# Kernel optimization log

Hardware: AMD Instinct MI355X
Metric: run time of the kernel (lower is better)

Reference implementation:

```python
import jax, jax.numpy as jnp
import numpy as np

N_NODES = 50000
N_EDGES = 600000
D = 128
EPS = 1e-5


def setup_inputs() -> dict:
    key = jax.random.key(0)
    ks = jax.random.split(key, 12)
    s = 1.0 / np.sqrt(D)
    return {
        "h": jax.random.normal(ks[0], (N_NODES, D), dtype=jnp.float32),
        "src": jax.random.randint(ks[1], (N_EDGES,), 0, N_NODES),
        "dst": jax.random.randint(ks[2], (N_EDGES,), 0, N_NODES),
        "W_pre": jax.random.uniform(ks[3], (D, D), jnp.float32, -s, s),
        "b_pre": jax.random.uniform(ks[4], (D,), jnp.float32, -s, s),
        "W1": jax.random.uniform(ks[5], (D, D), jnp.float32, -s, s),
        "b1": jax.random.uniform(ks[6], (D,), jnp.float32, -s, s),
        "W2": jax.random.uniform(ks[7], (D, D), jnp.float32, -s, s),
        "b2": jax.random.uniform(ks[8], (D,), jnp.float32, -s, s),
        "gamma": jnp.ones((D,), jnp.float32),
        "beta": jnp.zeros((D,), jnp.float32),
    }


def layer_norm(x, gamma, beta):
    mu = jnp.mean(x, axis=-1, keepdims=True)
    var = jnp.mean(jnp.square(x - mu), axis=-1, keepdims=True)
    return (x - mu) * jax.lax.rsqrt(var + EPS) * gamma + beta


def reference(h, src, dst, W_pre, b_pre, W1, b1, W2, b2, gamma, beta):
    # pre-projection: [N, D]
    h = h @ W_pre + b_pre
    # message passing: gather from src, segment-sum at dst (copy_u + sum)
    agg = jax.ops.segment_sum(h[src], dst, num_segments=N_NODES)
    # MLP (dropout is identity in eval)
    h_new = jax.nn.relu(jax.nn.relu(agg @ W1 + b1) @ W2 + b2)
    # residual + LayerNorm
    return layer_norm(h + h_new, gamma, beta)
```

## Files before the change

### kernel.cpp

```cpp
#include <hip/hip_runtime.h>

#define D 128
#define EPS 1e-5f
#define SCAN_CHUNK 1024
#define TSTRIDE 136

typedef __attribute__((ext_vector_type(8))) short bf16x8;
typedef __attribute__((ext_vector_type(4))) float floatx4;

__device__ __forceinline__ unsigned short f2bf(float f) {
    union { float f; unsigned u; } v; v.f = f;
    unsigned r = v.u + 0x7fffu + ((v.u >> 16) & 1u);
    return (unsigned short)(r >> 16);
}
__device__ __forceinline__ float bf2f(unsigned short s) {
    union { unsigned u; float f; } v; v.u = ((unsigned)s) << 16; return v.f;
}

__global__ __launch_bounds__(256) void prep(const float* __restrict__ W0,
                                            const float* __restrict__ W1,
                                            const float* __restrict__ W2,
                                            unsigned short* __restrict__ wt,
                                            int* __restrict__ counts, int nN) {
    int idx = blockIdx.x * 256 + threadIdx.x;
    if (idx < 3 * D * D) {
        int w = idx >> 14;
        int r = idx & (D * D - 1);
        int f = r >> 7, k = r & (D - 1);
        const float* W = (w == 0) ? W0 : (w == 1) ? W1 : W2;
        wt[(size_t)w * D * D + (size_t)f * D + k] = f2bf(W[(size_t)k * D + f]);
    }
    if (idx < nN) counts[idx] = 0;
}

__global__ __launch_bounds__(256) void hist_dst(const int* __restrict__ dst,
                                                int* __restrict__ counts, int nE) {
    int e = blockIdx.x * 256 + threadIdx.x;
    if (e < nE) atomicAdd(&counts[dst[e]], 1);
}

__global__ __launch_bounds__(256) void scan_chunk_sums(const int* __restrict__ counts,
                                                       int* __restrict__ chunkSums, int n) {
    __shared__ int sh[256];
    const int t = threadIdx.x;
    const int base = blockIdx.x * SCAN_CHUNK + t * 4;
    int s = 0;
#pragma unroll
    for (int i = 0; i < 4; ++i) {
        int idx = base + i;
        if (idx < n) s += counts[idx];
    }
    sh[t] = s;
    __syncthreads();
    for (int off = 128; off > 0; off >>= 1) {
        if (t < off) sh[t] += sh[t + off];
        __syncthreads();
    }
    if (t == 0) chunkSums[blockIdx.x] = sh[0];
}

__global__ __launch_bounds__(64) void scan_top(int* __restrict__ chunkSums, int nChunks,
                                               int* __restrict__ offsets, int nN, int nE) {
    const int t = threadIdx.x;
    int orig = (t < nChunks) ? chunkSums[t] : 0;
    int v = orig;
#pragma unroll
    for (int off = 1; off < 64; off <<= 1) {
        int u = __shfl_up(v, off, 64);
        if (t >= off) v += u;
    }
    if (t < nChunks) chunkSums[t] = v - orig;
    if (t == 0) offsets[nN] = nE;
}

__global__ __launch_bounds__(256) void scan_final(const int* __restrict__ counts,
                                                  const int* __restrict__ chunkSums,
                                                  int* __restrict__ offsets,
                                                  int* __restrict__ cursor, int n) {
    __shared__ int sh[256];
    const int t = threadIdx.x;
    const int base = blockIdx.x * SCAN_CHUNK + t * 4;
    int c[4];
    int s = 0;
#pragma unroll
    for (int i = 0; i < 4; ++i) {
        int idx = base + i;
        c[i] = (idx < n) ? counts[idx] : 0;
        s += c[i];
    }
    sh[t] = s;
    __syncthreads();
    int val = s;
    for (int off = 1; off < 256; off <<= 1) {
        int u = (t >= off) ? sh[t - off] : 0;
        __syncthreads();
        val += u;
        sh[t] = val;
        __syncthreads();
    }
    int run = val - s + chunkSums[blockIdx.x];
#pragma unroll
    for (int i = 0; i < 4; ++i) {
        int idx = base + i;
        if (idx < n) {
            offsets[idx] = run;
            cursor[idx] = run;
        }
        run += c[i];
    }
}

__global__ __launch_bounds__(256) void fill_edges(const int* __restrict__ src,
                                                  const int* __restrict__ dst,
                                                  int* __restrict__ cursor,
                                                  int* __restrict__ edge_src, int nE) {
    int e = blockIdx.x * 256 + threadIdx.x;
    if (e < nE) {
        int pos = atomicAdd(&cursor[dst[e]], 1);
        edge_src[pos] = src[e];
    }
}

__global__ __launch_bounds__(256) void gemm1(const float* __restrict__ X,
                                             const unsigned short* __restrict__ Wt,
                                             const float* __restrict__ bias,
                                             unsigned short* __restrict__ Y, int nrows) {
    const int t = threadIdx.x;
    const int lane = t & 63, wave = t >> 6;
    const int g = wave >> 1, hf = wave & 1;
    const int ml = lane & 15, q = lane >> 4;
    const int node = blockIdx.x * 32 + g * 16 + ml;
    const int rr = (node < nrows) ? node : (nrows - 1);
    const bool ok = (node < nrows);

    bf16x8 bfrag[4];
    const float* xp = X + (size_t)rr * D + q * 8;
#pragma unroll
    for (int kb = 0; kb < 4; ++kb) {
        float4 f0 = *(const float4*)(xp + kb * 32);
        float4 f1 = *(const float4*)(xp + kb * 32 + 4);
        bf16x8 v;
        v[0] = (short)f2bf(f0.x); v[1] = (short)f2bf(f0.y);
        v[2] = (short)f2bf(f0.z); v[3] = (short)f2bf(f0.w);
        v[4] = (short)f2bf(f1.x); v[5] = (short)f2bf(f1.y);
        v[6] = (short)f2bf(f1.z); v[7] = (short)f2bf(f1.w);
        bfrag[kb] = v;
    }

#pragma unroll
    for (int tl2 = 0; tl2 < 4; ++tl2) {
        const int tl = hf * 4 + tl2;
        floatx4 acc = {0.f, 0.f, 0.f, 0.f};
        const unsigned short* wp = Wt + (size_t)(tl * 16 + ml) * D + q * 8;
#pragma unroll
        for (int kb = 0; kb < 4; ++kb) {
            bf16x8 af = *(const bf16x8*)(wp + kb * 32);
            acc = __builtin_amdgcn_mfma_f32_16x16x32_bf16(af, bfrag[kb], acc, 0, 0, 0);
        }
        const int f0i = tl * 16 + q * 4;
        float4 b4 = *(const float4*)(bias + f0i);
        if (ok) {
            ushort4 o;
            o.x = f2bf(acc[0] + b4.x); o.y = f2bf(acc[1] + b4.y);
            o.z = f2bf(acc[2] + b4.z); o.w = f2bf(acc[3] + b4.w);
            *(ushort4*)(Y + (size_t)node * D + f0i) = o;
        }
    }
}

__global__ __launch_bounds__(256) void gather_sum(const unsigned short* __restrict__ hpre,
                                                  const int* __restrict__ offsets,
                                                  const int* __restrict__ edge_src,
                                                  unsigned short* __restrict__ agg, int nN) {
    const int t = threadIdx.x;
    const int li = t & 15;
    const int n = blockIdx.x * 16 + (t >> 4);
    if (n >= nN) return;
    const int beg = offsets[n], end = offsets[n + 1];

    float a[8] = {0.f, 0.f, 0.f, 0.f, 0.f, 0.f, 0.f, 0.f};
    int j = beg;
    int s0 = 0, s1 = 0;
    if (j < end) s0 = edge_src[j];
    if (j + 1 < end) s1 = edge_src[j + 1];

    while (j + 1 < end) {
        const int c0 = s0, c1 = s1;
        const int jn = j + 2;
        if (jn < end) s0 = edge_src[jn];
        if (jn + 1 < end) s1 = edge_src[jn + 1];
        bf16x8 v0 = *(const bf16x8*)(hpre + (size_t)c0 * D + li * 8);
        bf16x8 v1 = *(const bf16x8*)(hpre + (size_t)c1 * D + li * 8);
#pragma unroll
        for (int i = 0; i < 8; ++i)
            a[i] += bf2f((unsigned short)v0[i]) + bf2f((unsigned short)v1[i]);
        j = jn;
    }
    if (j < end) {
        bf16x8 v0 = *(const bf16x8*)(hpre + (size_t)s0 * D + li * 8);
#pragma unroll
        for (int i = 0; i < 8; ++i) a[i] += bf2f((unsigned short)v0[i]);
    }

    bf16x8 p;
#pragma unroll
    for (int i = 0; i < 8; ++i) p[i] = (short)f2bf(a[i]);
    *(bf16x8*)(agg + (size_t)n * D + li * 8) = p;
}

__global__ __launch_bounds__(256) void fused_mlp(const unsigned short* __restrict__ agg,
                                                 const unsigned short* __restrict__ hpre,
                                                 const unsigned short* __restrict__ Wt1,
                                                 const float* __restrict__ b1,
                                                 const unsigned short* __restrict__ Wt2,
                                                 const float* __restrict__ b2,
                                                 const float* __restrict__ gamma,
                                                 const float* __restrict__ beta,
                                                 float* __restrict__ out, int nN) {
    __shared__ unsigned short tile[32 * TSTRIDE];
    __shared__ float psm[2][32], psq[2][32];
    const int t = threadIdx.x;
    const int lane = t & 63, wave = t >> 6;
    const int g = wave >> 1, hf = wave & 1;
    const int ml = lane & 15, q = lane >> 4;
    const int lr = g * 16 + ml;
    const int node = blockIdx.x * 32 + lr;
    const int rr = (node < nN) ? node : (nN - 1);
    const bool ok = (node < nN);

    {
        bf16x8 bfrag[4];
        const unsigned short* xp = agg + (size_t)rr * D + q * 8;
#pragma unroll
        for (int kb = 0; kb < 4; ++kb) bfrag[kb] = *(const bf16x8*)(xp + kb * 32);

#pragma unroll
        for (int tl2 = 0; tl2 < 4; ++tl2) {
            const int tl = hf * 4 + tl2;
            floatx4 acc = {0.f, 0.f, 0.f, 0.f};
            const unsigned short* wp = Wt1 + (size_t)(tl * 16 + ml) * D + q * 8;
#pragma unroll
            for (int kb = 0; kb < 4; ++kb) {
                bf16x8 af = *(const bf16x8*)(wp + kb * 32);
                acc = __builtin_amdgcn_mfma_f32_16x16x32_bf16(af, bfrag[kb], acc, 0, 0, 0);
            }
            const int f0i = tl * 16 + q * 4;
            float4 b4 = *(const float4*)(b1 + f0i);
            ushort4 o;
            o.x = f2bf(fmaxf(acc[0] + b4.x, 0.f));
            o.y = f2bf(fmaxf(acc[1] + b4.y, 0.f));
            o.z = f2bf(fmaxf(acc[2] + b4.z, 0.f));
            o.w = f2bf(fmaxf(acc[3] + b4.w, 0.f));
            *(ushort4*)(&tile[lr * TSTRIDE + f0i]) = o;
        }
    }
    __syncthreads();

    float vs[4][4];
    float sm = 0.f, sq = 0.f;
    {
        bf16x8 bfrag[4];
#pragma unroll
        for (int kb = 0; kb < 4; ++kb)
            bfrag[kb] = *(const bf16x8*)(&tile[lr * TSTRIDE + kb * 32 + q * 8]);

#pragma unroll
        for (int tl2 = 0; tl2 < 4; ++tl2) {
            const int tl = hf * 4 + tl2;
            floatx4 acc = {0.f, 0.f, 0.f, 0.f};
            const unsigned short* wp = Wt2 + (size_t)(tl * 16 + ml) * D + q * 8;
#pragma unroll
            for (int kb = 0; kb < 4; ++kb) {
                bf16x8 af = *(const bf16x8*)(wp + kb * 32);
                acc = __builtin_amdgcn_mfma_f32_16x16x32_bf16(af, bfrag[kb], acc, 0, 0, 0);
            }
            const int f0i = tl * 16 + q * 4;
            float4 b4 = *(const float4*)(b2 + f0i);
            ushort4 hr = ((const ushort4*)(hpre + (size_t)rr * D + f0i))[0];
            float a0 = fmaxf(acc[0] + b4.x, 0.f) + bf2f(hr.x);
            float a1 = fmaxf(acc[1] + b4.y, 0.f) + bf2f(hr.y);
            float a2 = fmaxf(acc[2] + b4.z, 0.f) + bf2f(hr.z);
            float a3 = fmaxf(acc[3] + b4.w, 0.f) + bf2f(hr.w);
            vs[tl2][0] = a0; vs[tl2][1] = a1; vs[tl2][2] = a2; vs[tl2][3] = a3;
            sm += a0 + a1 + a2 + a3;
            sq += a0 * a0 + a1 * a1 + a2 * a2 + a3 * a3;
        }
        sm += __shfl_xor(sm, 16); sm += __shfl_xor(sm, 32);
        sq += __shfl_xor(sq, 16); sq += __shfl_xor(sq, 32);
        if (lane < 16) { psm[hf][lr] = sm; psq[hf][lr] = sq; }
    }
    __syncthreads();

    {
        const float smT = psm[0][lr] + psm[1][lr];
        const float sqT = psq[0][lr] + psq[1][lr];
        const float mu = smT * (1.f / D);
        const float var = sqT * (1.f / D) - mu * mu;
        const float is = rsqrtf(var + EPS);

        if (ok) {
#pragma unroll
            for (int tl2 = 0; tl2 < 4; ++tl2) {
                const int f0i = (hf * 4 + tl2) * 16 + q * 4;
                float4 g4 = *(const float4*)(gamma + f0i);
                float4 be4 = *(const float4*)(beta + f0i);
                float4 o;
                o.x = (vs[tl2][0] - mu) * is * g4.x + be4.x;
                o.y = (vs[tl2][1] - mu) * is * g4.y + be4.y;
                o.z = (vs[tl2][2] - mu) * is * g4.z + be4.z;
                o.w = (vs[tl2][3] - mu) * is * g4.w + be4.w;
                *(float4*)(out + (size_t)node * D + f0i) = o;
            }
        }
    }
}

extern "C" void kernel_launch(void* const* d_in, const int* in_sizes, int n_in,
                              void* d_out, int out_size, void* d_ws, size_t ws_size,
                              hipStream_t stream) {
    const float* h     = (const float*)d_in[0];
    const int*   src   = (const int*)d_in[1];
    const int*   dst   = (const int*)d_in[2];
    const float* W_pre = (const float*)d_in[3];
    const float* b_pre = (const float*)d_in[4];
    const float* W1    = (const float*)d_in[5];
    const float* b1    = (const float*)d_in[6];
    const float* W2    = (const float*)d_in[7];
    const float* b2    = (const float*)d_in[8];
    const float* gamma = (const float*)d_in[9];
    const float* beta  = (const float*)d_in[10];
    float* out = (float*)d_out;

    const int nN = in_sizes[0] / D;
    const int nE = in_sizes[1];
    const size_t rowsz = (size_t)nN * D;

    unsigned short* hpre = (unsigned short*)d_ws;
    unsigned short* agg  = hpre + rowsz;
    unsigned short* wt   = agg + rowsz;
    int* edge_src  = (int*)(wt + 3 * D * D);
    int* offsets   = edge_src + nE;
    int* cursor    = offsets + nN + 1;
    int* counts    = cursor + nN;
    int* chunkSums = counts + nN;

    const int prep_n  = (3 * D * D > nN) ? 3 * D * D : nN;
    const int eblocks = (nE + 255) / 256;
    const int gblocks = (nN + 31) / 32;
    const int nChunks = (nN + SCAN_CHUNK - 1) / SCAN_CHUNK;

    prep<<<(prep_n + 255) / 256, 256, 0, stream>>>(W_pre, W1, W2, wt, counts, nN);
    hist_dst<<<eblocks, 256, 0, stream>>>(dst, counts, nE);
    scan_chunk_sums<<<nChunks, 256, 0, stream>>>(counts, chunkSums, nN);
    scan_top<<<1, 64, 0, stream>>>(chunkSums, nChunks, offsets, nN, nE);
    scan_final<<<nChunks, 256, 0, stream>>>(counts, chunkSums, offsets, cursor, nN);
    fill_edges<<<eblocks, 256, 0, stream>>>(src, dst, cursor, edge_src, nE);

    gemm1<<<gblocks, 256, 0, stream>>>(h, wt, b_pre, hpre, nN);
    gather_sum<<<(nN + 15) / 16, 256, 0, stream>>>(hpre, offsets, edge_src, agg, nN);
    fused_mlp<<<gblocks, 256, 0, stream>>>(agg, hpre, wt + D * D, b1, wt + 2 * D * D, b2,
                                           gamma, beta, out, nN);
}
```

Baseline: 243.3 us.

## Fold scan_top into scan_final and double rows per block in GEMM kernels

Removes the single-block scan_top launch. Each scan_final block now computes the chunk-prefix with a wave shuffle scan, and prep writes offsets[nN]. The gemm1 and fused_mlp kernels each process 64 rows per block instead of 32. Each weight fragment is reused across two MFMA calls, which halves weight reloads per row and halves the block count, at the cost of more registers and LDS per block.

```diff
diff --git a/kernel.cpp b/kernel.cpp
--- a/kernel.cpp
+++ b/kernel.cpp
@@ -21,7 +21,8 @@
                                             const float* __restrict__ W1,
                                             const float* __restrict__ W2,
                                             unsigned short* __restrict__ wt,
-                                            int* __restrict__ counts, int nN) {
+                                            int* __restrict__ counts,
+                                            int* __restrict__ offsets, int nN, int nE) {
     int idx = blockIdx.x * 256 + threadIdx.x;
     if (idx < 3 * D * D) {
         int w = idx >> 14;
@@ -31,6 +32,7 @@
         wt[(size_t)w * D * D + (size_t)f * D + k] = f2bf(W[(size_t)k * D + f]);
     }
     if (idx < nN) counts[idx] = 0;
+    if (idx == 0) offsets[nN] = nE;
 }
 
 __global__ __launch_bounds__(256) void hist_dst(const int* __restrict__ dst,
@@ -59,26 +61,24 @@
     if (t == 0) chunkSums[blockIdx.x] = sh[0];
 }
 
-__global__ __launch_bounds__(64) void scan_top(int* __restrict__ chunkSums, int nChunks,
-                                               int* __restrict__ offsets, int nN, int nE) {
-    const int t = threadIdx.x;
-    int orig = (t < nChunks) ? chunkSums[t] : 0;
-    int v = orig;
-#pragma unroll
-    for (int off = 1; off < 64; off <<= 1) {
-        int u = __shfl_up(v, off, 64);
-        if (t >= off) v += u;
-    }
-    if (t < nChunks) chunkSums[t] = v - orig;
-    if (t == 0) offsets[nN] = nE;
-}
-
 __global__ __launch_bounds__(256) void scan_final(const int* __restrict__ counts,
                                                   const int* __restrict__ chunkSums,
+                                                  int nChunks,
                                                   int* __restrict__ offsets,
                                                   int* __restrict__ cursor, int n) {
     __shared__ int sh[256];
+    __shared__ int sbase;
     const int t = threadIdx.x;
+    if (t < 64) {
+        int orig = (t < nChunks) ? chunkSums[t] : 0;
+        int v = orig;
+#pragma unroll
+        for (int off = 1; off < 64; off <<= 1) {
+            int u = __shfl_up(v, off, 64);
+            if (t >= off) v += u;
+        }
+        if (t == blockIdx.x) sbase = v - orig;
+    }
     const int base = blockIdx.x * SCAN_CHUNK + t * 4;
     int c[4];
     int s = 0;
@@ -98,7 +98,7 @@
         sh[t] = val;
         __syncthreads();
     }
-    int run = val - s + chunkSums[blockIdx.x];
+    int run = val - s + sbase;
 #pragma unroll
     for (int i = 0; i < 4; ++i) {
         int idx = base + i;
@@ -129,41 +129,60 @@
     const int lane = t & 63, wave = t >> 6;
     const int g = wave >> 1, hf = wave & 1;
     const int ml = lane & 15, q = lane >> 4;
-    const int node = blockIdx.x * 32 + g * 16 + ml;
-    const int rr = (node < nrows) ? node : (nrows - 1);
-    const bool ok = (node < nrows);
-
-    bf16x8 bfrag[4];
-    const float* xp = X + (size_t)rr * D + q * 8;
-#pragma unroll
-    for (int kb = 0; kb < 4; ++kb) {
-        float4 f0 = *(const float4*)(xp + kb * 32);
-        float4 f1 = *(const float4*)(xp + kb * 32 + 4);
-        bf16x8 v;
-        v[0] = (short)f2bf(f0.x); v[1] = (short)f2bf(f0.y);
-        v[2] = (short)f2bf(f0.z); v[3] = (short)f2bf(f0.w);
-        v[4] = (short)f2bf(f1.x); v[5] = (short)f2bf(f1.y);
-        v[6] = (short)f2bf(f1.z); v[7] = (short)f2bf(f1.w);
-        bfrag[kb] = v;
+    const int n0 = blockIdx.x * 64 + g * 32 + ml;
+    const int n1 = n0 + 16;
+    const int rr0 = (n0 < nrows) ? n0 : (nrows - 1);
+    const int rr1 = (n1 < nrows) ? n1 : (nrows - 1);
+    const bool ok0 = (n0 < nrows), ok1 = (n1 < nrows);
+
+    bf16x8 bf0[4], bf1[4];
+    {
+        const float* x0 = X + (size_t)rr0 * D + q * 8;
+        const float* x1 = X + (size_t)rr1 * D + q * 8;
+#pragma unroll
+        for (int kb = 0; kb < 4; ++kb) {
+            float4 a0 = *(const float4*)(x0 + kb * 32);
+            float4 a1 = *(const float4*)(x0 + kb * 32 + 4);
+            float4 c0 = *(const float4*)(x1 + kb * 32);
+            float4 c1 = *(const float4*)(x1 + kb * 32 + 4);
+            bf16x8 v0, v1;
+            v0[0] = (short)f2bf(a0.x); v0[1] = (short)f2bf(a0.y);
+            v0[2] = (short)f2bf(a0.z); v0[3] = (short)f2bf(a0.w);
+            v0[4] = (short)f2bf(a1.x); v0[5] = (short)f2bf(a1.y);
+            v0[6] = (short)f2bf(a1.z); v0[7] = (short)f2bf(a1.w);
+            v1[0] = (short)f2bf(c0.x); v1[1] = (short)f2bf(c0.y);
+            v1[2] = (short)f2bf(c0.z); v1[3] = (short)f2bf(c0.w);
+            v1[4] = (short)f2bf(c1.x); v1[5] = (short)f2bf(c1.y);
+            v1[6] = (short)f2bf(c1.z); v1[7] = (short)f2bf(c1.w);
+            bf0[kb] = v0; bf1[kb] = v1;
+        }
     }
 
 #pragma unroll
     for (int tl2 = 0; tl2 < 4; ++tl2) {
         const int tl = hf * 4 + tl2;
-        floatx4 acc = {0.f, 0.f, 0.f, 0.f};
+        floatx4 ac0 = {0.f, 0.f, 0.f, 0.f};
+        floatx4 ac1 = {0.f, 0.f, 0.f, 0.f};
         const unsigned short* wp = Wt + (size_t)(tl * 16 + ml) * D + q * 8;
 #pragma unroll
         for (int kb = 0; kb < 4; ++kb) {
             bf16x8 af = *(const bf16x8*)(wp + kb * 32);
-            acc = __builtin_amdgcn_mfma_f32_16x16x32_bf16(af, bfrag[kb], acc, 0, 0, 0);
+            ac0 = __builtin_amdgcn_mfma_f32_16x16x32_bf16(af, bf0[kb], ac0, 0, 0, 0);
+            ac1 = __builtin_amdgcn_mfma_f32_16x16x32_bf16(af, bf1[kb], ac1, 0, 0, 0);
         }
         const int f0i = tl * 16 + q * 4;
         float4 b4 = *(const float4*)(bias + f0i);
-        if (ok) {
+        if (ok0) {
             ushort4 o;
-            o.x = f2bf(acc[0] + b4.x); o.y = f2bf(acc[1] + b4.y);
-            o.z = f2bf(acc[2] + b4.z); o.w = f2bf(acc[3] + b4.w);
-            *(ushort4*)(Y + (size_t)node * D + f0i) = o;
+            o.x = f2bf(ac0[0] + b4.x); o.y = f2bf(ac0[1] + b4.y);
+            o.z = f2bf(ac0[2] + b4.z); o.w = f2bf(ac0[3] + b4.w);
+            *(ushort4*)(Y + (size_t)n0 * D + f0i) = o;
+        }
+        if (ok1) {
+            ushort4 o;
+            o.x = f2bf(ac1[0] + b4.x); o.y = f2bf(ac1[1] + b4.y);
+            o.z = f2bf(ac1[2] + b4.z); o.w = f2bf(ac1[3] + b4.w);
+            *(ushort4*)(Y + (size_t)n1 * D + f0i) = o;
         }
     }
 }
@@ -217,99 +236,140 @@
                                                  const float* __restrict__ gamma,
                                                  const float* __restrict__ beta,
                                                  float* __restrict__ out, int nN) {
-    __shared__ unsigned short tile[32 * TSTRIDE];
-    __shared__ float psm[2][32], psq[2][32];
+    __shared__ unsigned short tile[64 * TSTRIDE];
+    __shared__ float psm[2][64], psq[2][64];
     const int t = threadIdx.x;
     const int lane = t & 63, wave = t >> 6;
     const int g = wave >> 1, hf = wave & 1;
     const int ml = lane & 15, q = lane >> 4;
-    const int lr = g * 16 + ml;
-    const int node = blockIdx.x * 32 + lr;
-    const int rr = (node < nN) ? node : (nN - 1);
-    const bool ok = (node < nN);
+    const int lr0 = g * 32 + ml, lr1 = lr0 + 16;
+    const int n0 = blockIdx.x * 64 + lr0;
+    const int n1 = blockIdx.x * 64 + lr1;
+    const int rr0 = (n0 < nN) ? n0 : (nN - 1);
+    const int rr1 = (n1 < nN) ? n1 : (nN - 1);
+    const bool ok0 = (n0 < nN), ok1 = (n1 < nN);
 
     {
-        bf16x8 bfrag[4];
-        const unsigned short* xp = agg + (size_t)rr * D + q * 8;
-#pragma unroll
-        for (int kb = 0; kb < 4; ++kb) bfrag[kb] = *(const bf16x8*)(xp + kb * 32);
+        bf16x8 bf0[4], bf1[4];
+        const unsigned short* x0 = agg + (size_t)rr0 * D + q * 8;
+        const unsigned short* x1 = agg + (size_t)rr1 * D + q * 8;
+#pragma unroll
+        for (int kb = 0; kb < 4; ++kb) {
+            bf0[kb] = *(const bf16x8*)(x0 + kb * 32);
+            bf1[kb] = *(const bf16x8*)(x1 + kb * 32);
+        }
 
 #pragma unroll
         for (int tl2 = 0; tl2 < 4; ++tl2) {
             const int tl = hf * 4 + tl2;
-            floatx4 acc = {0.f, 0.f, 0.f, 0.f};
+            floatx4 ac0 = {0.f, 0.f, 0.f, 0.f};
+            floatx4 ac1 = {0.f, 0.f, 0.f, 0.f};
             const unsigned short* wp = Wt1 + (size_t)(tl * 16 + ml) * D + q * 8;
 #pragma unroll
             for (int kb = 0; kb < 4; ++kb) {
                 bf16x8 af = *(const bf16x8*)(wp + kb * 32);
-                acc = __builtin_amdgcn_mfma_f32_16x16x32_bf16(af, bfrag[kb], acc, 0, 0, 0);
+                ac0 = __builtin_amdgcn_mfma_f32_16x16x32_bf16(af, bf0[kb], ac0, 0, 0, 0);
+                ac1 = __builtin_amdgcn_mfma_f32_16x16x32_bf16(af, bf1[kb], ac1, 0, 0, 0);
             }
             const int f0i = tl * 16 + q * 4;
             float4 b4 = *(const float4*)(b1 + f0i);
-            ushort4 o;
-            o.x = f2bf(fmaxf(acc[0] + b4.x, 0.f));
-            o.y = f2bf(fmaxf(acc[1] + b4.y, 0.f));
-            o.z = f2bf(fmaxf(acc[2] + b4.z, 0.f));
-            o.w = f2bf(fmaxf(acc[3] + b4.w, 0.f));
-            *(ushort4*)(&tile[lr * TSTRIDE + f0i]) = o;
+            ushort4 o0, o1;
+            o0.x = f2bf(fmaxf(ac0[0] + b4.x, 0.f));
+            o0.y = f2bf(fmaxf(ac0[1] + b4.y, 0.f));
+            o0.z = f2bf(fmaxf(ac0[2] + b4.z, 0.f));
+            o0.w = f2bf(fmaxf(ac0[3] + b4.w, 0.f));
+            o1.x = f2bf(fmaxf(ac1[0] + b4.x, 0.f));
+            o1.y = f2bf(fmaxf(ac1[1] + b4.y, 0.f));
+            o1.z = f2bf(fmaxf(ac1[2] + b4.z, 0.f));
+            o1.w = f2bf(fmaxf(ac1[3] + b4.w, 0.f));
+            *(ushort4*)(&tile[lr0 * TSTRIDE + f0i]) = o0;
+            *(ushort4*)(&tile[lr1 * TSTRIDE + f0i]) = o1;
         }
     }
     __syncthreads();
 
-    float vs[4][4];
-    float sm = 0.f, sq = 0.f;
+    float vs0[4][4], vs1[4][4];
     {
-        bf16x8 bfrag[4];
-#pragma unroll
-        for (int kb = 0; kb < 4; ++kb)
-            bfrag[kb] = *(const bf16x8*)(&tile[lr * TSTRIDE + kb * 32 + q * 8]);
-
+        bf16x8 bf0[4], bf1[4];
+#pragma unroll
+        for (int kb = 0; kb < 4; ++kb) {
+            bf0[kb] = *(const bf16x8*)(&tile[lr0 * TSTRIDE + kb * 32 + q * 8]);
+            bf1[kb] = *(const bf16x8*)(&tile[lr1 * TSTRIDE + kb * 32 + q * 8]);
+        }
+
+        float sm0 = 0.f, sq0 = 0.f, sm1 = 0.f, sq1 = 0.f;
 #pragma unroll
         for (int tl2 = 0; tl2 < 4; ++tl2) {
             const int tl = hf * 4 + tl2;
-            floatx4 acc = {0.f, 0.f, 0.f, 0.f};
+            floatx4 ac0 = {0.f, 0.f, 0.f, 0.f};
+            floatx4 ac1 = {0.f, 0.f, 0.f, 0.f};
             const unsigned short* wp = Wt2 + (size_t)(tl * 16 + ml) * D + q * 8;
 #pragma unroll
             for (int kb = 0; kb < 4; ++kb) {
                 bf16x8 af = *(const bf16x8*)(wp + kb * 32);
-                acc = __builtin_amdgcn_mfma_f32_16x16x32_bf16(af, bfrag[kb], acc, 0, 0, 0);
+                ac0 = __builtin_amdgcn_mfma_f32_16x16x32_bf16(af, bf0[kb], ac0, 0, 0, 0);
+                ac1 = __builtin_amdgcn_mfma_f32_16x16x32_bf16(af, bf1[kb], ac1, 0, 0, 0);
             }
             const int f0i = tl * 16 + q * 4;
             float4 b4 = *(const float4*)(b2 + f0i);
-            ushort4 hr = ((const ushort4*)(hpre + (size_t)rr * D + f0i))[0];
-            float a0 = fmaxf(acc[0] + b4.x, 0.f) + bf2f(hr.x);
-            float a1 = fmaxf(acc[1] + b4.y, 0.f) + bf2f(hr.y);
-            float a2 = fmaxf(acc[2] + b4.z, 0.f) + bf2f(hr.z);
-            float a3 = fmaxf(acc[3] + b4.w, 0.f) + bf2f(hr.w);
-            vs[tl2][0] = a0; vs[tl2][1] = a1; vs[tl2][2] = a2; vs[tl2][3] = a3;
-            sm += a0 + a1 + a2 + a3;
-            sq += a0 * a0 + a1 * a1 + a2 * a2 + a3 * a3;
-        }
-        sm += __shfl_xor(sm, 16); sm += __shfl_xor(sm, 32);
-        sq += __shfl_xor(sq, 16); sq += __shfl_xor(sq, 32);
-        if (lane < 16) { psm[hf][lr] = sm; psq[hf][lr] = sq; }
+            ushort4 h0 = ((const ushort4*)(hpre + (size_t)rr0 * D + f0i))[0];
+            ushort4 h1 = ((const ushort4*)(hpre + (size_t)rr1 * D + f0i))[0];
+            float a0 = fmaxf(ac0[0] + b4.x, 0.f) + bf2f(h0.x);
+            float a1 = fmaxf(ac0[1] + b4.y, 0.f) + bf2f(h0.y);
+            float a2 = fmaxf(ac0[2] + b4.z, 0.f) + bf2f(h0.z);
+            float a3 = fmaxf(ac0[3] + b4.w, 0.f) + bf2f(h0.w);
+            float c0 = fmaxf(ac1[0] + b4.x, 0.f) + bf2f(h1.x);
+            float c1 = fmaxf(ac1[1] + b4.y, 0.f) + bf2f(h1.y);
+            float c2 = fmaxf(ac1[2] + b4.z, 0.f) + bf2f(h1.z);
+            float c3 = fmaxf(ac1[3] + b4.w, 0.f) + bf2f(h1.w);
+            vs0[tl2][0] = a0; vs0[tl2][1] = a1; vs0[tl2][2] = a2; vs0[tl2][3] = a3;
+            vs1[tl2][0] = c0; vs1[tl2][1] = c1; vs1[tl2][2] = c2; vs1[tl2][3] = c3;
+            sm0 += a0 + a1 + a2 + a3;
+            sq0 += a0 * a0 + a1 * a1 + a2 * a2 + a3 * a3;
+            sm1 += c0 + c1 + c2 + c3;
+            sq1 += c0 * c0 + c1 * c1 + c2 * c2 + c3 * c3;
+        }
+        sm0 += __shfl_xor(sm0, 16); sm0 += __shfl_xor(sm0, 32);
+        sq0 += __shfl_xor(sq0, 16); sq0 += __shfl_xor(sq0, 32);
+        sm1 += __shfl_xor(sm1, 16); sm1 += __shfl_xor(sm1, 32);
+        sq1 += __shfl_xor(sq1, 16); sq1 += __shfl_xor(sq1, 32);
+        if (lane < 16) {
+            psm[hf][lr0] = sm0; psq[hf][lr0] = sq0;
+            psm[hf][lr1] = sm1; psq[hf][lr1] = sq1;
+        }
     }
     __syncthreads();
 
     {
-        const float smT = psm[0][lr] + psm[1][lr];
-        const float sqT = psq[0][lr] + psq[1][lr];
-        const float mu = smT * (1.f / D);
-        const float var = sqT * (1.f / D) - mu * mu;
-        const float is = rsqrtf(var + EPS);
-
-        if (ok) {
-#pragma unroll
-            for (int tl2 = 0; tl2 < 4; ++tl2) {
-                const int f0i = (hf * 4 + tl2) * 16 + q * 4;
-                float4 g4 = *(const float4*)(gamma + f0i);
-                float4 be4 = *(const float4*)(beta + f0i);
+        const float smT0 = psm[0][lr0] + psm[1][lr0];
+        const float sqT0 = psq[0][lr0] + psq[1][lr0];
+        const float smT1 = psm[0][lr1] + psm[1][lr1];
+        const float sqT1 = psq[0][lr1] + psq[1][lr1];
+        const float mu0 = smT0 * (1.f / D);
+        const float is0 = rsqrtf(sqT0 * (1.f / D) - mu0 * mu0 + EPS);
+        const float mu1 = smT1 * (1.f / D);
+        const float is1 = rsqrtf(sqT1 * (1.f / D) - mu1 * mu1 + EPS);
+
+#pragma unroll
+        for (int tl2 = 0; tl2 < 4; ++tl2) {
+            const int f0i = (hf * 4 + tl2) * 16 + q * 4;
+            float4 g4 = *(const float4*)(gamma + f0i);
+            float4 be4 = *(const float4*)(beta + f0i);
+            if (ok0) {
                 float4 o;
-                o.x = (vs[tl2][0] - mu) * is * g4.x + be4.x;
-                o.y = (vs[tl2][1] - mu) * is * g4.y + be4.y;
-                o.z = (vs[tl2][2] - mu) * is * g4.z + be4.z;
-                o.w = (vs[tl2][3] - mu) * is * g4.w + be4.w;
-                *(float4*)(out + (size_t)node * D + f0i) = o;
+                o.x = (vs0[tl2][0] - mu0) * is0 * g4.x + be4.x;
+                o.y = (vs0[tl2][1] - mu0) * is0 * g4.y + be4.y;
+                o.z = (vs0[tl2][2] - mu0) * is0 * g4.z + be4.z;
+                o.w = (vs0[tl2][3] - mu0) * is0 * g4.w + be4.w;
+                *(float4*)(out + (size_t)n0 * D + f0i) = o;
+            }
+            if (ok1) {
+                float4 o;
+                o.x = (vs1[tl2][0] - mu1) * is1 * g4.x + be4.x;
+                o.y = (vs1[tl2][1] - mu1) * is1 * g4.y + be4.y;
+                o.z = (vs1[tl2][2] - mu1) * is1 * g4.z + be4.z;
+                o.w = (vs1[tl2][3] - mu1) * is1 * g4.w + be4.w;
+                *(float4*)(out + (size_t)n1 * D + f0i) = o;
             }
         }
     }
@@ -346,14 +406,13 @@
 
     const int prep_n  = (3 * D * D > nN) ? 3 * D * D : nN;
     const int eblocks = (nE + 255) / 256;
-    const int gblocks = (nN + 31) / 32;
+    const int gblocks = (nN + 63) / 64;
     const int nChunks = (nN + SCAN_CHUNK - 1) / SCAN_CHUNK;
 
-    prep<<<(prep_n + 255) / 256, 256, 0, stream>>>(W_pre, W1, W2, wt, counts, nN);
+    prep<<<(prep_n + 255) / 256, 256, 0, stream>>>(W_pre, W1, W2, wt, counts, offsets, nN, nE);
     hist_dst<<<eblocks, 256, 0, stream>>>(dst, counts, nE);
     scan_chunk_sums<<<nChunks, 256, 0, stream>>>(counts, chunkSums, nN);
-    scan_top<<<1, 64, 0, stream>>>(chunkSums, nChunks, offsets, nN, nE);
-    scan_final<<<nChunks, 256, 0, stream>>>(counts, chunkSums, offsets, cursor, nN);
+    scan_final<<<nChunks, 256, 0, stream>>>(counts, chunkSums, nChunks, offsets, cursor, nN);
     fill_edges<<<eblocks, 256, 0, stream>>>(src, dst, cursor, edge_src, nE);
 
     gemm1<<<gblocks, 256, 0, stream>>>(h, wt, b_pre, hpre, nN);
```

Result: faster. 227.5 us (-6.5%).
